# Kernel tuning notes

Measured on AMD Instinct MI355X. Metric: run time of the kernel, lower is better.

Reference implementation:

```python
import jax, jax.numpy as jnp
import numpy as np

B, L, E, H = 2, 2048, 1024, 16
D = E // H


def _complex_linear(xr, xi, Wr, Wi, br, bi):
    # (xr + i*xi) @ (Wr + i*Wi)^T + (br + i*bi)
    yr = xr @ Wr.T - xi @ Wi.T + br
    yi = xr @ Wi.T + xi @ Wr.T + bi
    return yr, yi


def _split_heads(x):
    # [B, L, E] -> [B, H, L, D]
    return x.reshape(B, -1, H, D).transpose(0, 2, 1, 3)


def setup_inputs() -> dict:
    key = jax.random.key(0)
    ks = jax.random.split(key, 32)
    s = 1.0 / np.sqrt(E)
    inp = {}
    names = ["query_r", "query_i", "key_r", "key_i", "value_r", "value_i"]
    for i, n in enumerate(names):
        inp[n] = jax.random.normal(ks[i], (B, L, E), dtype=jnp.float32)
    j = 6
    for p in ["q", "k", "v", "o"]:
        inp[f"W{p}_r"] = jax.random.normal(ks[j], (E, E), dtype=jnp.float32) * s; j += 1
        inp[f"W{p}_i"] = jax.random.normal(ks[j], (E, E), dtype=jnp.float32) * s; j += 1
        inp[f"b{p}_r"] = jax.random.normal(ks[j], (E,), dtype=jnp.float32) * 0.01; j += 1
        inp[f"b{p}_i"] = jax.random.normal(ks[j], (E,), dtype=jnp.float32) * 0.01; j += 1
    return inp


def reference(query_r, query_i, key_r, key_i, value_r, value_i,
              Wq_r, Wq_i, bq_r, bq_i,
              Wk_r, Wk_i, bk_r, bk_i,
              Wv_r, Wv_i, bv_r, bv_i,
              Wo_r, Wo_i, bo_r, bo_i):
    qr, qi = _complex_linear(query_r, query_i, Wq_r, Wq_i, bq_r, bq_i)
    kr, ki = _complex_linear(key_r, key_i, Wk_r, Wk_i, bk_r, bk_i)
    vr, vi = _complex_linear(value_r, value_i, Wv_r, Wv_i, bv_r, bv_i)
    qr, qi = _split_heads(qr), _split_heads(qi)
    kr, ki = _split_heads(kr), _split_heads(ki)
    vr, vi = _split_heads(vr), _split_heads(vi)
    scale = jnp.float32(1.0 / np.sqrt(D))
    # Re(q @ conj(k)^T) = qr.kr^T + qi.ki^T  (imag part of scores is discarded)
    scores = (jnp.einsum('bhld,bhmd->bhlm', qr, kr)
              + jnp.einsum('bhld,bhmd->bhlm', qi, ki)) * scale
    probs = jax.nn.softmax(scores, axis=-1)  # real probs
    out_r = jnp.einsum('bhlm,bhmd->bhld', probs, vr)
    out_i = jnp.einsum('bhlm,bhmd->bhld', probs, vi)
    out_r = out_r.transpose(0, 2, 1, 3).reshape(B, L, E)
    out_i = out_i.transpose(0, 2, 1, 3).reshape(B, L, E)
    yr, yi = _complex_linear(out_r, out_i, Wo_r, Wo_i, bo_r, bo_i)
    return jnp.stack([yr, yi])  # [2, B, L, E] = (real, imag)
```

## Files before the change

kernel.cpp:

```cpp
#include <hip/hip_runtime.h>


#define LL 2048
#define EE 1024
#define HH 16
#define BL 4096
#define KK 2048

typedef __attribute__((ext_vector_type(8))) short bf16x8;
typedef __attribute__((ext_vector_type(4))) float f32x4;
typedef unsigned short u16;

__device__ __forceinline__ u16 f2bf(float x) {
    unsigned u = __builtin_bit_cast(unsigned, x);
    u += 0x7fff + ((u >> 16) & 1);
    return (u16)(u >> 16);
}

__device__ __forceinline__ void gl2lds16(const void* g, void* l) {
    __builtin_amdgcn_global_load_lds((const __attribute__((address_space(1))) void*)g,
                                     (__attribute__((address_space(3))) void*)l, 16, 0, 0);
}

struct ConvXArgs { const float* src[6]; u16* dst[6]; };
__global__ void conv_x(ConvXArgs a) {
    const int z = blockIdx.y;
    int i = blockIdx.x * 256 + threadIdx.x;
    float4 v = ((const float4*)a.src[z])[i];
    ushort4 o;
    o.x = f2bf(v.x); o.y = f2bf(v.y); o.z = f2bf(v.z); o.w = f2bf(v.w);
    ((ushort4*)a.dst[z])[i] = o;
}

struct ConvWArgs { const float* wr[4]; const float* wi[4]; u16* w2[4]; };
__global__ void conv_w(ConvWArgs a) {
    const int z = blockIdx.y;
    int i = blockIdx.x * 256 + threadIdx.x;
    int n = i >> 9, k = (i & 511) << 2;
    bool nh = n >= EE, kh = k >= EE;
    int nn = n & (EE - 1), kk = k & (EE - 1);
    const float* src = nh ? (kh ? a.wr[z] : a.wi[z]) : (kh ? a.wi[z] : a.wr[z]);
    float sgn = (!nh && kh) ? -1.0f : 1.0f;
    float4 v = *(const float4*)(src + nn * EE + kk);
    ushort4 o;
    o.x = f2bf(v.x * sgn); o.y = f2bf(v.y * sgn);
    o.z = f2bf(v.z * sgn); o.w = f2bf(v.w * sgn);
    *(ushort4*)(a.w2[z] + n * KK + k) = o;
}

struct QKVArgs {
    const u16* Ar[3]; const u16* Ai[3]; const u16* B2[3];
    const float* br[3]; const float* bi[3];
    u16* out[3];
    float oscale[3];
};

__launch_bounds__(256, 3)
__global__ void gemm_qkv(QKVArgs args) {
    __shared__ __attribute__((aligned(16))) u16 As[128 * 32];
    __shared__ __attribute__((aligned(16))) u16 Bs[128 * 32];

    const int z = blockIdx.z;
    const u16* __restrict__ Ar = args.Ar[z];
    const u16* __restrict__ Ai = args.Ai[z];
    const u16* __restrict__ B2 = args.B2[z];

    const int tid = threadIdx.x, wave = tid >> 6, lane = tid & 63;
    const int quad = lane >> 4, l16 = lane & 15;
    const int m0 = blockIdx.y * 128, n0 = blockIdx.x * 128;
    const int wm = (wave >> 1) * 64, wn = (wave & 1) * 64;
    const int srow = lane >> 2, scl = lane & 3;

    f32x4 acc[4][4] = {};

    for (int k0 = 0; k0 < KK; k0 += 32) {
        const u16* Asrc = (k0 < EE) ? (Ar + k0) : (Ai + (k0 - EE));
        const u16* Bsrc = B2 + k0;
        __syncthreads();
        for (int t = 0; t < 2; t++) {
            int r0 = (wave * 2 + t) * 16 + srow;
            int cg = scl ^ ((r0 >> 1) & 3);
            gl2lds16(Asrc + (m0 + r0) * EE + cg * 8, &As[(wave * 2 + t) * 512]);
            gl2lds16(Bsrc + (n0 + r0) * KK + cg * 8, &Bs[(wave * 2 + t) * 512]);
        }
        __syncthreads();
        bf16x8 a[4], b[4];
        for (int t = 0; t < 4; t++) {
            int ra = wm + t * 16 + l16;
            a[t] = *(const bf16x8*)&As[ra * 32 + ((quad ^ ((ra >> 1) & 3)) << 3)];
            int rb = wn + t * 16 + l16;
            b[t] = *(const bf16x8*)&Bs[rb * 32 + ((quad ^ ((rb >> 1) & 3)) << 3)];
        }
        for (int i = 0; i < 4; i++)
            for (int j = 0; j < 4; j++)
                acc[i][j] = __builtin_amdgcn_mfma_f32_16x16x32_bf16(a[i], b[j], acc[i][j], 0, 0, 0);
    }

    const float* __restrict__ br_ = args.br[z];
    const float* __restrict__ bi_ = args.bi[z];
    u16* __restrict__ out = args.out[z];
    const float oscale = args.oscale[z];

    for (int j = 0; j < 4; j++) {
        int gn = n0 + wn + j * 16 + l16;
        int ri = gn >> 10, e = gn & 1023;
        float bias = ri ? bi_[e] : br_[e];
        for (int i = 0; i < 4; i++) {
            int gmb = m0 + wm + i * 16 + quad * 4;
            for (int r = 0; r < 4; r++) {
                int gm = gmb + r;
                float v = (acc[i][j][r] + bias) * oscale;
                int b = gm >> 11, l = gm & 2047;
                int h = e >> 6, d = e & 63;
                if (z < 2)
                    out[((b * HH + h) * LL + l) * 128 + ri * 64 + d] = f2bf(v);
                else
                    out[((b * HH + h) * 128 + ri * 64 + d) * LL + l] = f2bf(v);
            }
        }
    }
}

__launch_bounds__(256, 2)
__global__ void gemm_oproj(const u16* __restrict__ Ar, const u16* __restrict__ Ai,
                           const u16* __restrict__ B2,
                           const float* __restrict__ br, const float* __restrict__ bi,
                           float* __restrict__ out)
{
    __shared__ __attribute__((aligned(16))) u16 As[128 * 32];
    __shared__ __attribute__((aligned(16))) u16 Bs[128 * 32];

    const int tid = threadIdx.x, wave = tid >> 6, lane = tid & 63;
    const int quad = lane >> 4, l16 = lane & 15;
    const int m0 = blockIdx.y * 128, n0 = blockIdx.x * 128;
    const int wm = (wave >> 1) * 64, wn = (wave & 1) * 64;
    const int srow = lane >> 2, scl = lane & 3;

    f32x4 acc[4][4] = {};

    for (int k0 = 0; k0 < KK; k0 += 32) {
        const u16* Asrc = (k0 < EE) ? (Ar + k0) : (Ai + (k0 - EE));
        const u16* Bsrc = B2 + k0;
        __syncthreads();
        for (int t = 0; t < 2; t++) {
            int r0 = (wave * 2 + t) * 16 + srow;
            int cg = scl ^ ((r0 >> 1) & 3);
            gl2lds16(Asrc + (m0 + r0) * EE + cg * 8, &As[(wave * 2 + t) * 512]);
            gl2lds16(Bsrc + (n0 + r0) * KK + cg * 8, &Bs[(wave * 2 + t) * 512]);
        }
        __syncthreads();
        bf16x8 a[4], b[4];
        for (int t = 0; t < 4; t++) {
            int ra = wm + t * 16 + l16;
            a[t] = *(const bf16x8*)&As[ra * 32 + ((quad ^ ((ra >> 1) & 3)) << 3)];
            int rb = wn + t * 16 + l16;
            b[t] = *(const bf16x8*)&Bs[rb * 32 + ((quad ^ ((rb >> 1) & 3)) << 3)];
        }
        for (int i = 0; i < 4; i++)
            for (int j = 0; j < 4; j++)
                acc[i][j] = __builtin_amdgcn_mfma_f32_16x16x32_bf16(a[i], b[j], acc[i][j], 0, 0, 0);
    }

    for (int j = 0; j < 4; j++) {
        int gn = n0 + wn + j * 16 + l16;
        int ri = gn >> 10, e = gn & 1023;
        float bias = ri ? bi[e] : br[e];
        for (int i = 0; i < 4; i++) {
            int gmb = m0 + wm + i * 16 + quad * 4;
            for (int r = 0; r < 4; r++) {
                int gm = gmb + r;
                out[ri * (BL * EE) + gm * EE + e] = acc[i][j][r] + bias;
            }
        }
    }
}

__launch_bounds__(256, 2)
__global__ void attn(const u16* __restrict__ q_ws, const u16* __restrict__ k_ws,
                     const u16* __restrict__ v_ws,
                     u16* __restrict__ o_r, u16* __restrict__ o_i)
{
    __shared__ __attribute__((aligned(16))) u16 kbuf[2][64 * 128];
    __shared__ __attribute__((aligned(16))) u16 vbuf[128 * 64];
    __shared__ __attribute__((aligned(16))) float red_sh[4][32];

    const int tid = threadIdx.x, wave = tid >> 6, lane = tid & 63;
    const int quad = lane >> 4, l16 = lane & 15;
    const int q0 = blockIdx.x * 128, bh = blockIdx.y;

    bf16x8 qf[2][4];
    for (int ntq = 0; ntq < 2; ntq++) {
        const u16* qp = q_ws + (size_t)(bh * LL + q0 + wave * 32 + ntq * 16 + l16) * 128 + quad * 8;
        for (int ks = 0; ks < 4; ks++)
            qf[ntq][ks] = *(const bf16x8*)(qp + ks * 32);
    }

    auto stage_k = [&](int nb, int kv0) {
        for (int t = 0; t < 4; t++) {
            int s = wave * 4 + t;
            int row = s * 4 + (lane >> 4);
            int cg = (lane & 15) ^ (row & 15);
            gl2lds16(k_ws + (size_t)(bh * LL + kv0 + row) * 128 + cg * 8, &kbuf[nb][s * 512]);
        }
    };
    auto stage_v = [&](int kv0) {
        for (int t = 0; t < 4; t++) {
            int s = wave * 4 + t;
            int row = s * 8 + (lane >> 3);
            int cg = (lane & 7) ^ (row & 7);
            gl2lds16(v_ws + (size_t)(bh * 128 + row) * LL + kv0 + cg * 8, &vbuf[s * 512]);
        }
    };

    stage_k(0, 0);
    stage_v(0);
    stage_k(1, 64);
    __syncthreads();

    f32x4 oacc[2][8] = {};
    float m_st[2] = {-__builtin_inff(), -__builtin_inff()};
    float l_st[2] = {0.f, 0.f};

    for (int N = 0; N < 32; N++) {
        const int cur = N & 1;
        u16* K = kbuf[cur];

        f32x4 s[4][2] = {};
        for (int ks = 0; ks < 4; ks++) {
            bf16x8 kf[4];
            for (int mt = 0; mt < 4; mt++) {
                int row = mt * 16 + l16;
                int cl = (ks * 4 + quad) ^ (row & 15);
                kf[mt] = *(const bf16x8*)&K[row * 128 + cl * 8];
            }
            for (int mt = 0; mt < 4; mt++)
                for (int ntq = 0; ntq < 2; ntq++)
                    s[mt][ntq] = __builtin_amdgcn_mfma_f32_16x16x32_bf16(kf[mt], qf[ntq][ks], s[mt][ntq], 0, 0, 0);
        }

        bool changed = false;
        float alpha[2];
        for (int ntq = 0; ntq < 2; ntq++) {
            float mx = -__builtin_inff();
            for (int mt = 0; mt < 4; mt++)
                for (int r = 0; r < 4; r++)
                    mx = fmaxf(mx, s[mt][ntq][r]);
            mx = fmaxf(mx, __shfl_xor(mx, 16, 64));
            mx = fmaxf(mx, __shfl_xor(mx, 32, 64));
            float mnew = fmaxf(m_st[ntq], mx);
            changed |= (mnew != m_st[ntq]);
            alpha[ntq] = __builtin_amdgcn_exp2f(m_st[ntq] - mnew);
            m_st[ntq] = mnew;
            float sum = 0.f;
            for (int mt = 0; mt < 4; mt++)
                for (int r = 0; r < 4; r++) {
                    float p = __builtin_amdgcn_exp2f(s[mt][ntq][r] - mnew);
                    s[mt][ntq][r] = p;
                    sum += p;
                }
            sum += __shfl_xor(sum, 16, 64);
            sum += __shfl_xor(sum, 32, 64);
            l_st[ntq] = l_st[ntq] * alpha[ntq] + sum;
            if (quad == 0) red_sh[wave][ntq * 16 + l16] = alpha[ntq];
        }
        __syncthreads();

        u16* P = kbuf[cur] + wave * 2048;
        for (int ntq = 0; ntq < 2; ntq++)
            for (int mt = 0; mt < 4; mt++) {
                int q = ntq * 16 + l16;
                int cg = mt * 2 + (quad >> 1);
                int cl = cg ^ (q & 7);
                ushort4 pk;
                pk.x = f2bf(s[mt][ntq][0]); pk.y = f2bf(s[mt][ntq][1]);
                pk.z = f2bf(s[mt][ntq][2]); pk.w = f2bf(s[mt][ntq][3]);
                *(ushort4*)&P[q * 64 + cl * 8 + (quad & 1) * 4] = pk;
            }

        if (__any(changed)) {
            f32x4 av[2];
            av[0] = *(const f32x4*)&red_sh[wave][quad * 4];
            av[1] = *(const f32x4*)&red_sh[wave][16 + quad * 4];
            for (int mtq = 0; mtq < 2; mtq++)
                for (int nt = 0; nt < 8; nt++)
                    oacc[mtq][nt] *= av[mtq];
        }

        for (int ks = 0; ks < 2; ks++) {
            bf16x8 pf[2];
            for (int mtq = 0; mtq < 2; mtq++) {
                int q = mtq * 16 + l16;
                int cl = (ks * 4 + quad) ^ (q & 7);
                pf[mtq] = *(const bf16x8*)&P[q * 64 + cl * 8];
            }
            for (int nt = 0; nt < 8; nt++) {
                int row = nt * 16 + l16;
                int cl = (ks * 4 + quad) ^ (row & 7);
                bf16x8 vf = *(const bf16x8*)&vbuf[row * 64 + cl * 8];
                for (int mtq = 0; mtq < 2; mtq++)
                    oacc[mtq][nt] = __builtin_amdgcn_mfma_f32_16x16x32_bf16(pf[mtq], vf, oacc[mtq][nt], 0, 0, 0);
            }
        }
        __syncthreads();

        if (N + 2 < 32) stage_k(cur, (N + 2) * 64);
        if (N + 1 < 32) stage_v((N + 1) * 64);
    }

    if (quad == 0) {
        red_sh[wave][l16] = l_st[0];
        red_sh[wave][16 + l16] = l_st[1];
    }
    __syncthreads();
    f32x4 lv[2];
    lv[0] = *(const f32x4*)&red_sh[wave][quad * 4];
    lv[1] = *(const f32x4*)&red_sh[wave][16 + quad * 4];
    const int b = bh >> 4, h = bh & 15;
    for (int mtq = 0; mtq < 2; mtq++) {
        f32x4 inv;
        for (int r = 0; r < 4; r++) inv[r] = 1.0f / lv[mtq][r];
        for (int nt = 0; nt < 8; nt++) {
            int d2 = nt * 16 + l16;
            u16* op = (d2 < 64) ? o_r : o_i;
            int col = h * 64 + (d2 & 63);
            for (int r = 0; r < 4; r++) {
                int l = q0 + wave * 32 + mtq * 16 + quad * 4 + r;
                op[(size_t)(b * LL + l) * EE + col] = f2bf(oacc[mtq][nt][r] * inv[r]);
            }
        }
    }
}

extern "C" void kernel_launch(void* const* d_in, const int* in_sizes, int n_in,
                              void* d_out, int out_size, void* d_ws, size_t ws_size,
                              hipStream_t stream) {
    const float* bq_r = (const float*)d_in[8];
    const float* bq_i = (const float*)d_in[9];
    const float* bk_r = (const float*)d_in[12];
    const float* bk_i = (const float*)d_in[13];
    const float* bv_r = (const float*)d_in[16];
    const float* bv_i = (const float*)d_in[17];
    const float* bo_r = (const float*)d_in[20];
    const float* bo_i = (const float*)d_in[21];

    u16* ws = (u16*)d_ws;
    const size_t XN = 4194304;
    u16* xqr = ws;            u16* xqi = xqr + XN;
    u16* xkr = xqi + XN;      u16* xki = xkr + XN;
    u16* xvr = xki + XN;      u16* xvi = xvr + XN;
    u16* w2q = xvi + XN;
    u16* w2k = w2q + XN;
    u16* w2v = w2k + XN;
    u16* w2o = w2v + XN;
    u16* q_ws = w2o + XN;
    u16* k_ws = q_ws + 8388608;
    u16* v_ws = k_ws + 8388608;
    u16* o_r = xqr;
    u16* o_i = xqr + XN;

    dim3 blk(256);

    ConvXArgs cx;
    cx.src[0] = (const float*)d_in[0]; cx.dst[0] = xqr;
    cx.src[1] = (const float*)d_in[1]; cx.dst[1] = xqi;
    cx.src[2] = (const float*)d_in[2]; cx.dst[2] = xkr;
    cx.src[3] = (const float*)d_in[3]; cx.dst[3] = xki;
    cx.src[4] = (const float*)d_in[4]; cx.dst[4] = xvr;
    cx.src[5] = (const float*)d_in[5]; cx.dst[5] = xvi;
    conv_x<<<dim3(4096, 6), blk, 0, stream>>>(cx);

    ConvWArgs cw;
    cw.wr[0] = (const float*)d_in[6];  cw.wi[0] = (const float*)d_in[7];  cw.w2[0] = w2q;
    cw.wr[1] = (const float*)d_in[10]; cw.wi[1] = (const float*)d_in[11]; cw.w2[1] = w2k;
    cw.wr[2] = (const float*)d_in[14]; cw.wi[2] = (const float*)d_in[15]; cw.w2[2] = w2v;
    cw.wr[3] = (const float*)d_in[18]; cw.wi[3] = (const float*)d_in[19]; cw.w2[3] = w2o;
    conv_w<<<dim3(4096, 4), blk, 0, stream>>>(cw);

    const float QSCALE = 0.125f * 1.44269504088896f;
    QKVArgs qa;
    qa.Ar[0] = xqr; qa.Ai[0] = xqi; qa.B2[0] = w2q; qa.br[0] = bq_r; qa.bi[0] = bq_i; qa.out[0] = q_ws; qa.oscale[0] = QSCALE;
    qa.Ar[1] = xkr; qa.Ai[1] = xki; qa.B2[1] = w2k; qa.br[1] = bk_r; qa.bi[1] = bk_i; qa.out[1] = k_ws; qa.oscale[1] = 1.0f;
    qa.Ar[2] = xvr; qa.Ai[2] = xvi; qa.B2[2] = w2v; qa.br[2] = bv_r; qa.bi[2] = bv_i; qa.out[2] = v_ws; qa.oscale[2] = 1.0f;
    gemm_qkv<<<dim3(16, 32, 3), blk, 0, stream>>>(qa);

    attn<<<dim3(16, 32), blk, 0, stream>>>(q_ws, k_ws, v_ws, o_r, o_i);

    gemm_oproj<<<dim3(16, 32), blk, 0, stream>>>(o_r, o_i, w2o, bo_r, bo_i, (float*)d_out);
}
```

Baseline: 479.8 us.

## Double GEMM K-tile to 64 and halve attention query tile per block

```diff
diff --git a/kernel.cpp b/kernel.cpp
--- a/kernel.cpp
+++ b/kernel.cpp
@@ -48,6 +48,35 @@
     *(ushort4*)(a.w2[z] + n * KK + k) = o;
 }
 
+#define GEMM_BK64_LOOP(Ar, Ai, B2)                                             \
+    for (int k0 = 0; k0 < KK; k0 += 64) {                                      \
+        const u16* Asrc = (k0 < EE) ? (Ar + k0) : (Ai + (k0 - EE));            \
+        const u16* Bsrc = B2 + k0;                                             \
+        __syncthreads();                                                       \
+        {                                                                      \
+            int rr = lane >> 3, cg = (lane & 7) ^ rr;                          \
+            for (int t = 0; t < 4; t++) {                                      \
+                int s = wave * 4 + t;                                          \
+                int r0 = s * 8 + rr;                                           \
+                gl2lds16(Asrc + (size_t)(m0 + r0) * EE + cg * 8, &As[s * 512]);\
+                gl2lds16(Bsrc + (size_t)(n0 + r0) * KK + cg * 8, &Bs[s * 512]);\
+            }                                                                  \
+        }                                                                      \
+        __syncthreads();                                                       \
+        for (int ks2 = 0; ks2 < 2; ks2++) {                                    \
+            bf16x8 a[4], b[4];                                                 \
+            for (int t = 0; t < 4; t++) {                                      \
+                int ra = wm + t * 16 + l16;                                    \
+                a[t] = *(const bf16x8*)&As[ra * 64 + (((ks2 * 4 + quad) ^ (ra & 7)) << 3)]; \
+                int rb = wn + t * 16 + l16;                                    \
+                b[t] = *(const bf16x8*)&Bs[rb * 64 + (((ks2 * 4 + quad) ^ (rb & 7)) << 3)]; \
+            }                                                                  \
+            for (int i = 0; i < 4; i++)                                        \
+                for (int j = 0; j < 4; j++)                                    \
+                    acc[i][j] = __builtin_amdgcn_mfma_f32_16x16x32_bf16(a[i], b[j], acc[i][j], 0, 0, 0); \
+        }                                                                      \
+    }
+
 struct QKVArgs {
     const u16* Ar[3]; const u16* Ai[3]; const u16* B2[3];
     const float* br[3]; const float* bi[3];
@@ -57,8 +86,8 @@
 
 __launch_bounds__(256, 3)
 __global__ void gemm_qkv(QKVArgs args) {
-    __shared__ __attribute__((aligned(16))) u16 As[128 * 32];
-    __shared__ __attribute__((aligned(16))) u16 Bs[128 * 32];
+    __shared__ __attribute__((aligned(16))) u16 As[128 * 64];
+    __shared__ __attribute__((aligned(16))) u16 Bs[128 * 64];
 
     const int z = blockIdx.z;
     const u16* __restrict__ Ar = args.Ar[z];
@@ -69,32 +98,10 @@
     const int quad = lane >> 4, l16 = lane & 15;
     const int m0 = blockIdx.y * 128, n0 = blockIdx.x * 128;
     const int wm = (wave >> 1) * 64, wn = (wave & 1) * 64;
-    const int srow = lane >> 2, scl = lane & 3;
 
     f32x4 acc[4][4] = {};
 
-    for (int k0 = 0; k0 < KK; k0 += 32) {
-        const u16* Asrc = (k0 < EE) ? (Ar + k0) : (Ai + (k0 - EE));
-        const u16* Bsrc = B2 + k0;
-        __syncthreads();
-        for (int t = 0; t < 2; t++) {
-            int r0 = (wave * 2 + t) * 16 + srow;
-            int cg = scl ^ ((r0 >> 1) & 3);
-            gl2lds16(Asrc + (m0 + r0) * EE + cg * 8, &As[(wave * 2 + t) * 512]);
-            gl2lds16(Bsrc + (n0 + r0) * KK + cg * 8, &Bs[(wave * 2 + t) * 512]);
-        }
-        __syncthreads();
-        bf16x8 a[4], b[4];
-        for (int t = 0; t < 4; t++) {
-            int ra = wm + t * 16 + l16;
-            a[t] = *(const bf16x8*)&As[ra * 32 + ((quad ^ ((ra >> 1) & 3)) << 3)];
-            int rb = wn + t * 16 + l16;
-            b[t] = *(const bf16x8*)&Bs[rb * 32 + ((quad ^ ((rb >> 1) & 3)) << 3)];
-        }
-        for (int i = 0; i < 4; i++)
-            for (int j = 0; j < 4; j++)
-                acc[i][j] = __builtin_amdgcn_mfma_f32_16x16x32_bf16(a[i], b[j], acc[i][j], 0, 0, 0);
-    }
+    GEMM_BK64_LOOP(Ar, Ai, B2)
 
     const float* __restrict__ br_ = args.br[z];
     const float* __restrict__ bi_ = args.bi[z];
@@ -127,39 +134,17 @@
                            const float* __restrict__ br, const float* __restrict__ bi,
                            float* __restrict__ out)
 {
-    __shared__ __attribute__((aligned(16))) u16 As[128 * 32];
-    __shared__ __attribute__((aligned(16))) u16 Bs[128 * 32];
+    __shared__ __attribute__((aligned(16))) u16 As[128 * 64];
+    __shared__ __attribute__((aligned(16))) u16 Bs[128 * 64];
 
     const int tid = threadIdx.x, wave = tid >> 6, lane = tid & 63;
     const int quad = lane >> 4, l16 = lane & 15;
     const int m0 = blockIdx.y * 128, n0 = blockIdx.x * 128;
     const int wm = (wave >> 1) * 64, wn = (wave & 1) * 64;
-    const int srow = lane >> 2, scl = lane & 3;
 
     f32x4 acc[4][4] = {};
 
-    for (int k0 = 0; k0 < KK; k0 += 32) {
-        const u16* Asrc = (k0 < EE) ? (Ar + k0) : (Ai + (k0 - EE));
-        const u16* Bsrc = B2 + k0;
-        __syncthreads();
-        for (int t = 0; t < 2; t++) {
-            int r0 = (wave * 2 + t) * 16 + srow;
-            int cg = scl ^ ((r0 >> 1) & 3);
-            gl2lds16(Asrc + (m0 + r0) * EE + cg * 8, &As[(wave * 2 + t) * 512]);
-            gl2lds16(Bsrc + (n0 + r0) * KK + cg * 8, &Bs[(wave * 2 + t) * 512]);
-        }
-        __syncthreads();
-        bf16x8 a[4], b[4];
-        for (int t = 0; t < 4; t++) {
-            int ra = wm + t * 16 + l16;
-            a[t] = *(const bf16x8*)&As[ra * 32 + ((quad ^ ((ra >> 1) & 3)) << 3)];
-            int rb = wn + t * 16 + l16;
-            b[t] = *(const bf16x8*)&Bs[rb * 32 + ((quad ^ ((rb >> 1) & 3)) << 3)];
-        }
-        for (int i = 0; i < 4; i++)
-            for (int j = 0; j < 4; j++)
-                acc[i][j] = __builtin_amdgcn_mfma_f32_16x16x32_bf16(a[i], b[j], acc[i][j], 0, 0, 0);
-    }
+    GEMM_BK64_LOOP(Ar, Ai, B2)
 
     for (int j = 0; j < 4; j++) {
         int gn = n0 + wn + j * 16 + l16;
@@ -175,24 +160,24 @@
     }
 }
 
-__launch_bounds__(256, 2)
+__launch_bounds__(256, 3)
 __global__ void attn(const u16* __restrict__ q_ws, const u16* __restrict__ k_ws,
                      const u16* __restrict__ v_ws,
                      u16* __restrict__ o_r, u16* __restrict__ o_i)
 {
     __shared__ __attribute__((aligned(16))) u16 kbuf[2][64 * 128];
     __shared__ __attribute__((aligned(16))) u16 vbuf[128 * 64];
-    __shared__ __attribute__((aligned(16))) float red_sh[4][32];
+    __shared__ __attribute__((aligned(16))) float red_sh[4][16];
 
     const int tid = threadIdx.x, wave = tid >> 6, lane = tid & 63;
     const int quad = lane >> 4, l16 = lane & 15;
-    const int q0 = blockIdx.x * 128, bh = blockIdx.y;
-
-    bf16x8 qf[2][4];
-    for (int ntq = 0; ntq < 2; ntq++) {
-        const u16* qp = q_ws + (size_t)(bh * LL + q0 + wave * 32 + ntq * 16 + l16) * 128 + quad * 8;
+    const int q0 = blockIdx.x * 64, bh = blockIdx.y;
+
+    bf16x8 qf[4];
+    {
+        const u16* qp = q_ws + (size_t)(bh * LL + q0 + wave * 16 + l16) * 128 + quad * 8;
         for (int ks = 0; ks < 4; ks++)
-            qf[ntq][ks] = *(const bf16x8*)(qp + ks * 32);
+            qf[ks] = *(const bf16x8*)(qp + ks * 32);
     }
 
     auto stage_k = [&](int nb, int kv0) {
@@ -217,15 +202,15 @@
     stage_k(1, 64);
     __syncthreads();
 
-    f32x4 oacc[2][8] = {};
-    float m_st[2] = {-__builtin_inff(), -__builtin_inff()};
-    float l_st[2] = {0.f, 0.f};
+    f32x4 oacc[8] = {};
+    float m_st = -__builtin_inff();
+    float l_st = 0.f;
 
     for (int N = 0; N < 32; N++) {
         const int cur = N & 1;
         u16* K = kbuf[cur];
 
-        f32x4 s[4][2] = {};
+        f32x4 s[4] = {};
         for (int ks = 0; ks < 4; ks++) {
             bf16x8 kf[4];
             for (int mt = 0; mt < 4; mt++) {
@@ -234,71 +219,61 @@
                 kf[mt] = *(const bf16x8*)&K[row * 128 + cl * 8];
             }
             for (int mt = 0; mt < 4; mt++)
-                for (int ntq = 0; ntq < 2; ntq++)
-                    s[mt][ntq] = __builtin_amdgcn_mfma_f32_16x16x32_bf16(kf[mt], qf[ntq][ks], s[mt][ntq], 0, 0, 0);
+                s[mt] = __builtin_amdgcn_mfma_f32_16x16x32_bf16(kf[mt], qf[ks], s[mt], 0, 0, 0);
         }
 
         bool changed = false;
-        float alpha[2];
-        for (int ntq = 0; ntq < 2; ntq++) {
+        float alpha;
+        {
             float mx = -__builtin_inff();
             for (int mt = 0; mt < 4; mt++)
                 for (int r = 0; r < 4; r++)
-                    mx = fmaxf(mx, s[mt][ntq][r]);
+                    mx = fmaxf(mx, s[mt][r]);
             mx = fmaxf(mx, __shfl_xor(mx, 16, 64));
             mx = fmaxf(mx, __shfl_xor(mx, 32, 64));
-            float mnew = fmaxf(m_st[ntq], mx);
-            changed |= (mnew != m_st[ntq]);
-            alpha[ntq] = __builtin_amdgcn_exp2f(m_st[ntq] - mnew);
-            m_st[ntq] = mnew;
+            float mnew = fmaxf(m_st, mx);
+            changed = (mnew != m_st);
+            alpha = __builtin_amdgcn_exp2f(m_st - mnew);
+            m_st = mnew;
             float sum = 0.f;
             for (int mt = 0; mt < 4; mt++)
                 for (int r = 0; r < 4; r++) {
-                    float p = __builtin_amdgcn_exp2f(s[mt][ntq][r] - mnew);
-                    s[mt][ntq][r] = p;
+                    float p = __builtin_amdgcn_exp2f(s[mt][r] - mnew);
+                    s[mt][r] = p;
                     sum += p;
                 }
             sum += __shfl_xor(sum, 16, 64);
             sum += __shfl_xor(sum, 32, 64);
-            l_st[ntq] = l_st[ntq] * alpha[ntq] + sum;
-            if (quad == 0) red_sh[wave][ntq * 16 + l16] = alpha[ntq];
+            l_st = l_st * alpha + sum;
+            if (quad == 0) red_sh[wave][l16] = alpha;
         }
         __syncthreads();
 
-        u16* P = kbuf[cur] + wave * 2048;
-        for (int ntq = 0; ntq < 2; ntq++)
-            for (int mt = 0; mt < 4; mt++) {
-                int q = ntq * 16 + l16;
-                int cg = mt * 2 + (quad >> 1);
-                int cl = cg ^ (q & 7);
-                ushort4 pk;
-                pk.x = f2bf(s[mt][ntq][0]); pk.y = f2bf(s[mt][ntq][1]);
-                pk.z = f2bf(s[mt][ntq][2]); pk.w = f2bf(s[mt][ntq][3]);
-                *(ushort4*)&P[q * 64 + cl * 8 + (quad & 1) * 4] = pk;
-            }
+        u16* P = kbuf[cur] + wave * 1024;
+        for (int mt = 0; mt < 4; mt++) {
+            int q = l16;
+            int cg = mt * 2 + (quad >> 1);
+            int cl = cg ^ (q & 7);
+            ushort4 pk;
+            pk.x = f2bf(s[mt][0]); pk.y = f2bf(s[mt][1]);
+            pk.z = f2bf(s[mt][2]); pk.w = f2bf(s[mt][3]);
+            *(ushort4*)&P[q * 64 + cl * 8 + (quad & 1) * 4] = pk;
+        }
 
         if (__any(changed)) {
-            f32x4 av[2];
-            av[0] = *(const f32x4*)&red_sh[wave][quad * 4];
-            av[1] = *(const f32x4*)&red_sh[wave][16 + quad * 4];
-            for (int mtq = 0; mtq < 2; mtq++)
-                for (int nt = 0; nt < 8; nt++)
-                    oacc[mtq][nt] *= av[mtq];
+            f32x4 av = *(const f32x4*)&red_sh[wave][quad * 4];
+            for (int nt = 0; nt < 8; nt++)
+                oacc[nt] *= av;
         }
 
         for (int ks = 0; ks < 2; ks++) {
-            bf16x8 pf[2];
-            for (int mtq = 0; mtq < 2; mtq++) {
-                int q = mtq * 16 + l16;
-                int cl = (ks * 4 + quad) ^ (q & 7);
-                pf[mtq] = *(const bf16x8*)&P[q * 64 + cl * 8];
-            }
+            int clp = (ks * 4 + quad) ^ (l16 & 7);
+            bf16x8 pf = *(const bf16x8*)&P[l16 * 64 + clp * 8];
             for (int nt = 0; nt < 8; nt++) {
                 int row = nt * 16 + l16;
                 int cl = (ks * 4 + quad) ^ (row & 7);
                 bf16x8 vf = *(const bf16x8*)&vbuf[row * 64 + cl * 8];
-                for (int mtq = 0; mtq < 2; mtq++)
-                    oacc[mtq][nt] = __builtin_amdgcn_mfma_f32_16x16x32_bf16(pf[mtq], vf, oacc[mtq][nt], 0, 0, 0);
+                oacc[nt] = __builtin_amdgcn_mfma_f32_16x16x32_bf16(pf, vf, oacc[nt], 0, 0, 0);
             }
         }
         __syncthreads();
@@ -307,26 +282,19 @@
         if (N + 1 < 32) stage_v((N + 1) * 64);
     }
 
-    if (quad == 0) {
-        red_sh[wave][l16] = l_st[0];
-        red_sh[wave][16 + l16] = l_st[1];
-    }
+    if (quad == 0) red_sh[wave][l16] = l_st;
     __syncthreads();
-    f32x4 lv[2];
-    lv[0] = *(const f32x4*)&red_sh[wave][quad * 4];
-    lv[1] = *(const f32x4*)&red_sh[wave][16 + quad * 4];
+    f32x4 lv = *(const f32x4*)&red_sh[wave][quad * 4];
+    f32x4 inv;
+    for (int r = 0; r < 4; r++) inv[r] = 1.0f / lv[r];
     const int b = bh >> 4, h = bh & 15;
-    for (int mtq = 0; mtq < 2; mtq++) {
-        f32x4 inv;
-        for (int r = 0; r < 4; r++) inv[r] = 1.0f / lv[mtq][r];
-        for (int nt = 0; nt < 8; nt++) {
-            int d2 = nt * 16 + l16;
-            u16* op = (d2 < 64) ? o_r : o_i;
-            int col = h * 64 + (d2 & 63);
-            for (int r = 0; r < 4; r++) {
-                int l = q0 + wave * 32 + mtq * 16 + quad * 4 + r;
-                op[(size_t)(b * LL + l) * EE + col] = f2bf(oacc[mtq][nt][r] * inv[r]);
-            }
+    for (int nt = 0; nt < 8; nt++) {
+        int d2 = nt * 16 + l16;
+        u16* op = (d2 < 64) ? o_r : o_i;
+        int col = h * 64 + (d2 & 63);
+        for (int r = 0; r < 4; r++) {
+            int l = q0 + wave * 16 + quad * 4 + r;
+            op[(size_t)(b * LL + l) * EE + col] = f2bf(oacc[nt][r] * inv[r]);
         }
     }
 }
@@ -383,7 +351,7 @@
     qa.Ar[2] = xvr; qa.Ai[2] = xvi; qa.B2[2] = w2v; qa.br[2] = bv_r; qa.bi[2] = bv_i; qa.out[2] = v_ws; qa.oscale[2] = 1.0f;
     gemm_qkv<<<dim3(16, 32, 3), blk, 0, stream>>>(qa);
 
-    attn<<<dim3(16, 32), blk, 0, stream>>>(q_ws, k_ws, v_ws, o_r, o_i);
+    attn<<<dim3(32, 32), blk, 0, stream>>>(q_ws, k_ws, v_ws, o_r, o_i);
 
     gemm_oproj<<<dim3(16, 32), blk, 0, stream>>>(o_r, o_i, w2o, bo_r, bo_i, (float*)d_out);
 }
```

After: 468.5 us. 1.02x faster.
